# Kernel optimization log

Measured on AMD Instinct MI355X. Metric: run time of the kernel, lower is better.

Reference implementation:

```python
import jax, jax.numpy as jnp
import numpy as np

EMBED = 1024
HEADS = 16
HEAD_DIM = EMBED // HEADS
HIDDEN = 4096
EPS = 1e-6


def _layer_norm(x, gamma, beta):
    mu = jnp.mean(x, axis=-1, keepdims=True)
    var = jnp.mean(jnp.square(x - mu), axis=-1, keepdims=True)
    return (x - mu) * jax.lax.rsqrt(var + EPS) * gamma + beta


def setup_inputs() -> dict:
    key = jax.random.key(0)
    ks = jax.random.split(key, 16)
    s = 1.0 / np.sqrt(EMBED)
    sh = 1.0 / np.sqrt(HIDDEN)
    return {
        "x": jax.random.normal(ks[0], (2, 2048, EMBED), dtype=jnp.float32),
        "Wq": jax.random.uniform(ks[1], (EMBED, EMBED), jnp.float32, -s, s),
        "bq": jnp.zeros((EMBED,), jnp.float32),
        "Wk": jax.random.uniform(ks[2], (EMBED, EMBED), jnp.float32, -s, s),
        "bk": jnp.zeros((EMBED,), jnp.float32),
        "Wv": jax.random.uniform(ks[3], (EMBED, EMBED), jnp.float32, -s, s),
        "bv": jnp.zeros((EMBED,), jnp.float32),
        "Wo": jax.random.uniform(ks[4], (EMBED, EMBED), jnp.float32, -s, s),
        "bo": jnp.zeros((EMBED,), jnp.float32),
        "ln1_g": jnp.ones((EMBED,), jnp.float32),
        "ln1_b": jnp.zeros((EMBED,), jnp.float32),
        "W1": jax.random.uniform(ks[5], (EMBED, HIDDEN), jnp.float32, -s, s),
        "b1": jnp.zeros((HIDDEN,), jnp.float32),
        "W2": jax.random.uniform(ks[6], (HIDDEN, EMBED), jnp.float32, -sh, sh),
        "b2": jnp.zeros((EMBED,), jnp.float32),
        "ln2_g": jnp.ones((EMBED,), jnp.float32),
        "ln2_b": jnp.zeros((EMBED,), jnp.float32),
    }


def reference(x, Wq, bq, Wk, bk, Wv, bv, Wo, bo, ln1_g, ln1_b, W1, b1, W2, b2, ln2_g, ln2_b):
    B, S, _ = x.shape
    # projections (weights stored as [in, out])
    q = (x @ Wq + bq).reshape(B, S, HEADS, HEAD_DIM)
    k = (x @ Wk + bk).reshape(B, S, HEADS, HEAD_DIM)
    v = (x @ Wv + bv).reshape(B, S, HEADS, HEAD_DIM)
    # scores: [B, H, S, S]
    scores = jnp.einsum('bqhd,bkhd->bhqk', q, k) / jnp.sqrt(jnp.float32(HEAD_DIM))
    attn = jax.nn.softmax(scores, axis=-1)
    ctx = jnp.einsum('bhqk,bkhd->bqhd', attn, v).reshape(B, S, EMBED)
    attn_out = ctx @ Wo + bo
    x1 = _layer_norm(x + attn_out, ln1_g, ln1_b)
    ffn = jax.nn.relu(x1 @ W1 + b1) @ W2 + b2
    return _layer_norm(x1 + ffn, ln2_g, ln2_b)
```

## Files before the change

### kernel.cpp

```cpp
#include <hip/hip_runtime.h>
#include <math.h>

#define EMBED 1024
#define HEADS 16
#define HDIM  64
#define HIDDEN 4096
#define BATCH 2
#define SEQ   2048
#define TOK   (BATCH * SEQ)

typedef _Float16 f16;
typedef f16 f16x8 __attribute__((ext_vector_type(8)));
typedef f16 f16x4 __attribute__((ext_vector_type(4)));
typedef f16 f16x2 __attribute__((ext_vector_type(2)));
typedef float f32x4 __attribute__((ext_vector_type(4)));
typedef float f32x16 __attribute__((ext_vector_type(16)));

__device__ __forceinline__ void gload16(const void* g, void* s) {
  __builtin_amdgcn_global_load_lds(
      (const __attribute__((address_space(1))) unsigned int*)g,
      (__attribute__((address_space(3))) unsigned int*)s, 16, 0, 0);
}

template<int A16, int RELU, int OUT16, int QKV>
__global__ __launch_bounds__(256, 2)
void gemm_f16(const void* __restrict__ Av, const f16* __restrict__ Wt,
              const float* __restrict__ bias0, const float* __restrict__ bias1,
              const float* __restrict__ bias2, void* __restrict__ Cv,
              int N, int K, int nbx) {
  __shared__ f16 As[512 * 8];
  __shared__ f16 Bs[512 * 8];
  const int tid = threadIdx.x;
  const int l = tid & 63, w = tid >> 6;
  const int g = l >> 4, ln = l & 15;
  int bid = blockIdx.x;
  const int cpx = gridDim.x >> 3;
  bid = (bid & 7) * cpx + (bid >> 3);
  const int m0 = (bid / nbx) << 7;
  const int n0 = (bid % nbx) << 7;
  const int wr = w >> 1, wc = w & 1;

  f32x4 acc[4][4] = {};

  for (int k0 = 0; k0 < K; k0 += 32) {
    if (A16) {
      const f16* A = (const f16*)Av;
#pragma unroll
      for (int p = 0; p < 2; ++p) {
        const int u0 = p * 256 + w * 64;
        const int ks = u0 >> 7;
        const int row = ((u0 + l) & 127) ^ ks;
        gload16(A + (size_t)(m0 + row) * K + k0 + ks * 8, (void*)&As[u0 * 8]);
      }
    } else {
      const float* A = (const float*)Av;
      const int ks = tid & 3;
      const int r0 = tid >> 2;
#pragma unroll
      for (int p = 0; p < 2; ++p) {
        const int row = r0 + p * 64;
        const float* src = A + (size_t)(m0 + row) * K + k0 + ks * 8;
        float4 f0 = *(const float4*)src;
        float4 f1 = *(const float4*)(src + 4);
        f16x8 hh;
        hh[0] = (f16)f0.x; hh[1] = (f16)f0.y; hh[2] = (f16)f0.z; hh[3] = (f16)f0.w;
        hh[4] = (f16)f1.x; hh[5] = (f16)f1.y; hh[6] = (f16)f1.z; hh[7] = (f16)f1.w;
        *(f16x8*)&As[(ks * 128 + (row ^ ks)) * 8] = hh;
      }
    }
#pragma unroll
    for (int p = 0; p < 2; ++p) {
      const int u0 = p * 256 + w * 64;
      const int ks = u0 >> 7;
      const int col = ((u0 + l) & 127) ^ ks;
      gload16(Wt + (size_t)(n0 + col) * K + k0 + ks * 8, (void*)&Bs[u0 * 8]);
    }
    __syncthreads();
    f16x8 af[4], bf[4];
#pragma unroll
    for (int m = 0; m < 4; ++m)
      af[m] = *(const f16x8*)&As[(g * 128 + ((wr * 64 + m * 16 + ln) ^ g)) * 8];
#pragma unroll
    for (int n = 0; n < 4; ++n)
      bf[n] = *(const f16x8*)&Bs[(g * 128 + ((wc * 64 + n * 16 + ln) ^ g)) * 8];
#pragma unroll
    for (int m = 0; m < 4; ++m)
#pragma unroll
      for (int n = 0; n < 4; ++n)
        acc[m][n] = __builtin_amdgcn_mfma_f32_16x16x32_f16(af[m], bf[n], acc[m][n], 0, 0, 0);
    __syncthreads();
  }

  const float* bp = bias0;
  int nbase = n0;
  float scale = 1.f;
  if (QKV) {
    const int seg = n0 >> 10;
    bp = (seg == 0) ? bias0 : (seg == 1) ? bias1 : bias2;
    nbase = n0 & 1023;
    if (seg == 0) scale = 0.125f * 1.44269504f;
  }
  float bv[4];
#pragma unroll
  for (int n = 0; n < 4; ++n) bv[n] = bp[nbase + wc * 64 + n * 16 + ln];
#pragma unroll
  for (int m = 0; m < 4; ++m)
#pragma unroll
    for (int n = 0; n < 4; ++n)
#pragma unroll
      for (int r = 0; r < 4; ++r) {
        float v = (acc[m][n][r] + bv[n]) * scale;
        if (RELU) v = fmaxf(v, 0.f);
        const size_t idx = (size_t)(m0 + wr * 64 + m * 16 + g * 4 + r) * N
                         + n0 + wc * 64 + n * 16 + ln;
        if (OUT16) ((f16*)Cv)[idx] = (f16)v;
        else       ((float*)Cv)[idx] = v;
      }
}

__device__ __forceinline__ unsigned kchunk(int key, int m) { return (unsigned)(m ^ (key & 7)); }

template<int BASE>
__device__ __forceinline__ f16x8 pack_frag(f32x16 p) {
  f16x8 r;
#pragma unroll
  for (int j = 0; j < 8; ++j) r[j] = (f16)p[BASE + j];
  return r;
}

#define VSTRIDE 68

__global__ __launch_bounds__(256, 2)
void attention(const f16* __restrict__ qkv, f16* __restrict__ ctx) {
  __shared__ f16 Ks[64 * 64];
  __shared__ f16 VT[64 * VSTRIDE];
  const int tid = threadIdx.x;
  const int l = tid & 63, w = tid >> 6;
  const int ln = l & 31, hi = l >> 5;
  const int bh = blockIdx.y, b = bh >> 4, h = bh & 15;
  const int q0 = blockIdx.x * 128;

  f16x8 qf[4];
  {
    const f16* qp = qkv + (size_t)(b * SEQ + q0 + w * 32 + ln) * 3072 + h * 64 + hi * 8;
#pragma unroll
    for (int kc = 0; kc < 4; ++kc) qf[kc] = *(const f16x8*)(qp + kc * 16);
  }

  f32x16 o0 = {}, o1 = {};
  float mrow = -1e30f, lrow = 0.f;

  const int skey = tid >> 3, sc = tid & 7;

  for (int kt = 0; kt < SEQ / 64; ++kt) {
    const size_t tb = (size_t)(b * SEQ + kt * 64) * 3072 + h * 64;
    f16x8 va = *(const f16x8*)(qkv + tb + 2048 + (size_t)skey * 3072 + sc * 8);
    f16x8 vb = *(const f16x8*)(qkv + tb + 2048 + (size_t)(32 + skey) * 3072 + sc * 8);
#pragma unroll
    for (int p = 0; p < 2; ++p) {
      const int key = p * 32 + skey;
      gload16(qkv + tb + 1024 + (size_t)key * 3072 + 8 * kchunk(key, sc),
              (void*)&Ks[(p * 256 + w * 64) * 8]);
    }
#pragma unroll
    for (int j = 0; j < 8; ++j) {
      const int d = sc * 8 + j;
      VT[d * VSTRIDE + skey] = va[j];
      VT[d * VSTRIDE + 32 + skey] = vb[j];
    }
    __syncthreads();

    f32x16 st0 = {}, st1 = {};
#pragma unroll
    for (int kc = 0; kc < 4; ++kc) {
      const int m = kc * 2 + hi;
      const f16x8 kf0 = *(const f16x8*)&Ks[(ln * 8 + (m ^ (ln & 7))) * 8];
      const f16x8 kf1 = *(const f16x8*)&Ks[((32 + ln) * 8 + (m ^ (ln & 7))) * 8];
      st0 = __builtin_amdgcn_mfma_f32_32x32x16_f16(kf0, qf[kc], st0, 0, 0, 0);
      st1 = __builtin_amdgcn_mfma_f32_32x32x16_f16(kf1, qf[kc], st1, 0, 0, 0);
    }

    float mt = st0[0];
#pragma unroll
    for (int r = 1; r < 16; ++r) mt = fmaxf(mt, st0[r]);
#pragma unroll
    for (int r = 0; r < 16; ++r) mt = fmaxf(mt, st1[r]);
    mt = fmaxf(mt, __shfl_xor(mt, 32));
    const float mn = fmaxf(mrow, mt);
    const float al = exp2f(mrow - mn);
    mrow = mn;
    float ps = 0.f;
#pragma unroll
    for (int r = 0; r < 16; ++r) { st0[r] = exp2f(st0[r] - mn); ps += st0[r]; }
#pragma unroll
    for (int r = 0; r < 16; ++r) { st1[r] = exp2f(st1[r] - mn); ps += st1[r]; }
    ps += __shfl_xor(ps, 32);
    lrow = lrow * al + ps;
#pragma unroll
    for (int r = 0; r < 16; ++r) { o0[r] *= al; o1[r] *= al; }

    f16x8 pf[4];
    pf[0] = pack_frag<0>(st0); pf[1] = pack_frag<8>(st0);
    pf[2] = pack_frag<0>(st1); pf[3] = pack_frag<8>(st1);

#pragma unroll
    for (int s = 0; s < 4; ++s) {
      const int k0a = 16 * s + 4 * hi;
      {
        const f16* p0 = &VT[ln * VSTRIDE + k0a];
        f16x4 x = *(const f16x4*)p0;
        f16x4 y = *(const f16x4*)(p0 + 8);
        f16x8 vf = __builtin_shufflevector(x, y, 0, 1, 2, 3, 4, 5, 6, 7);
        o0 = __builtin_amdgcn_mfma_f32_32x32x16_f16(vf, pf[s], o0, 0, 0, 0);
      }
      {
        const f16* p1 = &VT[(32 + ln) * VSTRIDE + k0a];
        f16x4 x = *(const f16x4*)p1;
        f16x4 y = *(const f16x4*)(p1 + 8);
        f16x8 vf = __builtin_shufflevector(x, y, 0, 1, 2, 3, 4, 5, 6, 7);
        o1 = __builtin_amdgcn_mfma_f32_32x32x16_f16(vf, pf[s], o1, 0, 0, 0);
      }
    }
    __syncthreads();
  }

  const float inv = 1.f / lrow;
  f16* cp = ctx + (size_t)(b * SEQ + q0 + w * 32 + ln) * EMBED + h * 64;
#pragma unroll
  for (int r = 0; r < 16; ++r) {
    const int drow = (r & 3) + 8 * (r >> 2) + 4 * hi;
    cp[drow] = (f16)(o0[r] * inv);
    cp[32 + drow] = (f16)(o1[r] * inv);
  }
}

template<int OUT16>
__global__ __launch_bounds__(256, 4)
void add_ln(const float* __restrict__ a, const float* __restrict__ r,
            const float* __restrict__ gam, const float* __restrict__ bet,
            float* __restrict__ out, f16* __restrict__ out16) {
  const int t = blockIdx.x;
  const int tid = threadIdx.x;
  const size_t base = (size_t)t * EMBED + tid * 4;
  float4 av = *(const float4*)(a + base);
  float4 rv = *(const float4*)(r + base);
  const float x0 = av.x + rv.x, x1 = av.y + rv.y;
  const float x2 = av.z + rv.z, x3 = av.w + rv.w;
  float s1 = x0 + x1 + x2 + x3;
  float s2 = x0 * x0 + x1 * x1 + x2 * x2 + x3 * x3;
  for (int off = 1; off < 64; off <<= 1) {
    s1 += __shfl_xor(s1, off);
    s2 += __shfl_xor(s2, off);
  }
  __shared__ float red[8];
  if ((tid & 63) == 0) { red[(tid >> 6) * 2] = s1; red[(tid >> 6) * 2 + 1] = s2; }
  __syncthreads();
  s1 = red[0] + red[2] + red[4] + red[6];
  s2 = red[1] + red[3] + red[5] + red[7];
  const float mu = s1 * (1.f / EMBED);
  const float var = s2 * (1.f / EMBED) - mu * mu;
  const float rstd = rsqrtf(var + 1e-6f);
  float4 gv = *(const float4*)(gam + tid * 4);
  float4 bv = *(const float4*)(bet + tid * 4);
  float4 ov;
  ov.x = (x0 - mu) * rstd * gv.x + bv.x;
  ov.y = (x1 - mu) * rstd * gv.y + bv.y;
  ov.z = (x2 - mu) * rstd * gv.z + bv.z;
  ov.w = (x3 - mu) * rstd * gv.w + bv.w;
  *(float4*)(out + base) = ov;
  if (OUT16) {
    f16x4 hh;
    hh[0] = (f16)ov.x; hh[1] = (f16)ov.y; hh[2] = (f16)ov.z; hh[3] = (f16)ov.w;
    *(f16x4*)(out16 + base) = hh;
  }
}

__global__ __launch_bounds__(256, 4)
void transpose_w(const float* __restrict__ in, f16* __restrict__ out,
                 int K, int N) {
  __shared__ float t[32][33];
  const int tid = threadIdx.x;
  const int k0 = blockIdx.y * 32, n0 = blockIdx.x * 32;
  {
    const int ky = tid >> 3, nx = (tid & 7) * 4;
    float4 f = *(const float4*)(in + (size_t)(k0 + ky) * N + n0 + nx);
    t[ky][nx] = f.x; t[ky][nx + 1] = f.y; t[ky][nx + 2] = f.z; t[ky][nx + 3] = f.w;
  }
  __syncthreads();
  const int ny = tid >> 3, kx = (tid & 7) * 4;
  f16x4 hh;
  hh[0] = (f16)t[kx][ny];     hh[1] = (f16)t[kx + 1][ny];
  hh[2] = (f16)t[kx + 2][ny]; hh[3] = (f16)t[kx + 3][ny];
  *(f16x4*)(out + (size_t)(n0 + ny) * K + k0 + kx) = hh;
}

extern "C" void kernel_launch(void* const* d_in, const int* in_sizes, int n_in,
                              void* d_out, int out_size, void* d_ws, size_t ws_size,
                              hipStream_t stream) {
  const float* x    = (const float*)d_in[0];
  const float* Wq   = (const float*)d_in[1];
  const float* bq   = (const float*)d_in[2];
  const float* Wk   = (const float*)d_in[3];
  const float* bk   = (const float*)d_in[4];
  const float* Wv   = (const float*)d_in[5];
  const float* bv   = (const float*)d_in[6];
  const float* Wo   = (const float*)d_in[7];
  const float* bo   = (const float*)d_in[8];
  const float* ln1g = (const float*)d_in[9];
  const float* ln1b = (const float*)d_in[10];
  const float* W1   = (const float*)d_in[11];
  const float* b1   = (const float*)d_in[12];
  const float* W2   = (const float*)d_in[13];
  const float* b2   = (const float*)d_in[14];
  const float* ln2g = (const float*)d_in[15];
  const float* ln2b = (const float*)d_in[16];
  float* out = (float*)d_out;

  char* ws = (char*)d_ws;
  const size_t MB = 1024 * 1024;
  f16*   WtQKV = (f16*)(ws);
  f16*   WtO   = (f16*)(ws + 6 * MB);
  f16*   Wt1   = (f16*)(ws + 8 * MB);
  f16*   Wt2   = (f16*)(ws + 16 * MB);
  f16*   qkv   = (f16*)(ws + 24 * MB);
  f16*   ctx   = (f16*)(ws + 48 * MB);
  float* ao    = (float*)(ws + 56 * MB);
  float* x1    = (float*)(ws + 72 * MB);
  f16*   x1h   = (f16*)(ws + 88 * MB);
  f16*   hid   = (f16*)(ws + 24 * MB);
  float* ffn   = ao;

  const dim3 blk(256);
  transpose_w<<<dim3(32, 32), blk, 0, stream>>>(Wq, WtQKV, 1024, 1024);
  transpose_w<<<dim3(32, 32), blk, 0, stream>>>(Wk, WtQKV + 1024 * 1024, 1024, 1024);
  transpose_w<<<dim3(32, 32), blk, 0, stream>>>(Wv, WtQKV + 2 * 1024 * 1024, 1024, 1024);
  transpose_w<<<dim3(32, 32), blk, 0, stream>>>(Wo, WtO, 1024, 1024);
  transpose_w<<<dim3(128, 32), blk, 0, stream>>>(W1, Wt1, 1024, 4096);
  transpose_w<<<dim3(32, 128), blk, 0, stream>>>(W2, Wt2, 4096, 1024);

  gemm_f16<0, 0, 1, 1><<<768, blk, 0, stream>>>(x, WtQKV, bq, bk, bv, qkv, 3072, 1024, 24);
  attention<<<dim3(16, 32), blk, 0, stream>>>(qkv, ctx);
  gemm_f16<1, 0, 0, 0><<<256, blk, 0, stream>>>(ctx, WtO, bo, nullptr, nullptr, ao, 1024, 1024, 8);
  add_ln<1><<<4096, blk, 0, stream>>>(x, ao, ln1g, ln1b, x1, x1h);
  gemm_f16<1, 1, 1, 0><<<1024, blk, 0, stream>>>(x1h, Wt1, b1, nullptr, nullptr, hid, 4096, 1024, 32);
  gemm_f16<1, 0, 0, 0><<<256, blk, 0, stream>>>(hid, Wt2, b2, nullptr, nullptr, ffn, 1024, 4096, 8);
  add_ln<0><<<4096, blk, 0, stream>>>(x1, ffn, ln2g, ln2b, out, nullptr);
}
```

Baseline: 502.0 us.

## Split-K the N=1024 GEMMs and fold partial sums plus bias into add+LayerNorm

The Wo and W2 projections only produce 256 tiles of 128x128, which underfills the GPU. They now run as split-K with 2 slices (512 blocks), and each slice writes fp32 partials to the workspace. The add_ln kernel sums the partials, the bias and the residual before normalising. It also merges the three QKV weight transposes into one launch, raises the launch-bounds occupancy hint from 2 to 3, and writes x1 into the output buffer instead of a separate workspace region. The cost is extra fp32 partial-sum traffic and possible register pressure from the higher occupancy target.

```diff
diff --git a/kernel.cpp b/kernel.cpp
--- a/kernel.cpp
+++ b/kernel.cpp
@@ -12,7 +12,6 @@
 typedef _Float16 f16;
 typedef f16 f16x8 __attribute__((ext_vector_type(8)));
 typedef f16 f16x4 __attribute__((ext_vector_type(4)));
-typedef f16 f16x2 __attribute__((ext_vector_type(2)));
 typedef float f32x4 __attribute__((ext_vector_type(4)));
 typedef float f32x16 __attribute__((ext_vector_type(16)));
 
@@ -22,8 +21,8 @@
       (__attribute__((address_space(3))) unsigned int*)s, 16, 0, 0);
 }
 
-template<int A16, int RELU, int OUT16, int QKV>
-__global__ __launch_bounds__(256, 2)
+template<int A16, int RELU, int OUT16, int QKV, int SPLITK>
+__global__ __launch_bounds__(256, 3)
 void gemm_f16(const void* __restrict__ Av, const f16* __restrict__ Wt,
               const float* __restrict__ bias0, const float* __restrict__ bias1,
               const float* __restrict__ bias2, void* __restrict__ Cv,
@@ -34,15 +33,20 @@
   const int l = tid & 63, w = tid >> 6;
   const int g = l >> 4, ln = l & 15;
   int bid = blockIdx.x;
-  const int cpx = gridDim.x >> 3;
+  int slice = 0;
+  if (SPLITK > 1) { slice = bid % SPLITK; bid /= SPLITK; }
+  const int ntiles = gridDim.x / SPLITK;
+  const int cpx = ntiles >> 3;
   bid = (bid & 7) * cpx + (bid >> 3);
   const int m0 = (bid / nbx) << 7;
   const int n0 = (bid % nbx) << 7;
   const int wr = w >> 1, wc = w & 1;
+  const int ksl = K / SPLITK;
+  const int kbeg = slice * ksl, kend = kbeg + ksl;
 
   f32x4 acc[4][4] = {};
 
-  for (int k0 = 0; k0 < K; k0 += 32) {
+  for (int k0 = kbeg; k0 < kend; k0 += 32) {
     if (A16) {
       const f16* A = (const f16*)Av;
 #pragma unroll
@@ -91,6 +95,21 @@
     __syncthreads();
   }
 
+  if (SPLITK > 1) {
+    float* P = (float*)Cv + (size_t)slice * TOK * N;
+#pragma unroll
+    for (int m = 0; m < 4; ++m)
+#pragma unroll
+      for (int n = 0; n < 4; ++n)
+#pragma unroll
+        for (int r = 0; r < 4; ++r) {
+          const size_t idx = (size_t)(m0 + wr * 64 + m * 16 + g * 4 + r) * N
+                           + n0 + wc * 64 + n * 16 + ln;
+          P[idx] = acc[m][n][r];
+        }
+    return;
+  }
+
   const float* bp = bias0;
   int nbase = n0;
   float scale = 1.f;
@@ -234,18 +253,22 @@
   }
 }
 
-template<int OUT16>
+template<int NP, int OUT16>
 __global__ __launch_bounds__(256, 4)
-void add_ln(const float* __restrict__ a, const float* __restrict__ r,
-            const float* __restrict__ gam, const float* __restrict__ bet,
-            float* __restrict__ out, f16* __restrict__ out16) {
+void add_ln(const float* parts, const float* __restrict__ bias,
+            const float* resid, const float* __restrict__ gam,
+            const float* __restrict__ bet, float* out, f16* __restrict__ out16) {
   const int t = blockIdx.x;
   const int tid = threadIdx.x;
   const size_t base = (size_t)t * EMBED + tid * 4;
-  float4 av = *(const float4*)(a + base);
-  float4 rv = *(const float4*)(r + base);
-  const float x0 = av.x + rv.x, x1 = av.y + rv.y;
-  const float x2 = av.z + rv.z, x3 = av.w + rv.w;
+  float4 rv = *(const float4*)(resid + base);
+  float4 bb = *(const float4*)(bias + tid * 4);
+  float x0 = rv.x + bb.x, x1 = rv.y + bb.y, x2 = rv.z + bb.z, x3 = rv.w + bb.w;
+#pragma unroll
+  for (int p = 0; p < NP; ++p) {
+    float4 pv = *(const float4*)(parts + (size_t)p * TOK * EMBED + base);
+    x0 += pv.x; x1 += pv.y; x2 += pv.z; x3 += pv.w;
+  }
   float s1 = x0 + x1 + x2 + x3;
   float s2 = x0 * x0 + x1 * x1 + x2 * x2 + x3 * x3;
   for (int off = 1; off < 64; off <<= 1) {
@@ -275,12 +298,9 @@
   }
 }
 
-__global__ __launch_bounds__(256, 4)
-void transpose_w(const float* __restrict__ in, f16* __restrict__ out,
-                 int K, int N) {
+__device__ __forceinline__ void transpose_tile(const float* in, f16* out,
+                                               int K, int N, int k0, int n0, int tid) {
   __shared__ float t[32][33];
-  const int tid = threadIdx.x;
-  const int k0 = blockIdx.y * 32, n0 = blockIdx.x * 32;
   {
     const int ky = tid >> 3, nx = (tid & 7) * 4;
     float4 f = *(const float4*)(in + (size_t)(k0 + ky) * N + n0 + nx);
@@ -292,6 +312,20 @@
   hh[0] = (f16)t[kx][ny];     hh[1] = (f16)t[kx + 1][ny];
   hh[2] = (f16)t[kx + 2][ny]; hh[3] = (f16)t[kx + 3][ny];
   *(f16x4*)(out + (size_t)(n0 + ny) * K + k0 + kx) = hh;
+}
+
+__global__ __launch_bounds__(256, 4)
+void transpose_w(const float* __restrict__ in, f16* __restrict__ out,
+                 int K, int N) {
+  transpose_tile(in, out, K, N, blockIdx.y * 32, blockIdx.x * 32, threadIdx.x);
+}
+
+__global__ __launch_bounds__(256, 4)
+void transpose_qkv(const float* __restrict__ w0, const float* __restrict__ w1,
+                   const float* __restrict__ w2, f16* __restrict__ out) {
+  const float* in = (blockIdx.z == 0) ? w0 : (blockIdx.z == 1) ? w1 : w2;
+  f16* o = out + (size_t)blockIdx.z * 1024 * 1024;
+  transpose_tile(in, o, 1024, 1024, blockIdx.y * 32, blockIdx.x * 32, threadIdx.x);
 }
 
 extern "C" void kernel_launch(void* const* d_in, const int* in_sizes, int n_in,
@@ -324,25 +358,22 @@
   f16*   Wt2   = (f16*)(ws + 16 * MB);
   f16*   qkv   = (f16*)(ws + 24 * MB);
   f16*   ctx   = (f16*)(ws + 48 * MB);
-  float* ao    = (float*)(ws + 56 * MB);
-  float* x1    = (float*)(ws + 72 * MB);
+  float* parts = (float*)(ws + 56 * MB);
   f16*   x1h   = (f16*)(ws + 88 * MB);
   f16*   hid   = (f16*)(ws + 24 * MB);
-  float* ffn   = ao;
+  float* x1    = out;
 
   const dim3 blk(256);
-  transpose_w<<<dim3(32, 32), blk, 0, stream>>>(Wq, WtQKV, 1024, 1024);
-  transpose_w<<<dim3(32, 32), blk, 0, stream>>>(Wk, WtQKV + 1024 * 1024, 1024, 1024);
-  transpose_w<<<dim3(32, 32), blk, 0, stream>>>(Wv, WtQKV + 2 * 1024 * 1024, 1024, 1024);
+  transpose_qkv<<<dim3(32, 32, 3), blk, 0, stream>>>(Wq, Wk, Wv, WtQKV);
   transpose_w<<<dim3(32, 32), blk, 0, stream>>>(Wo, WtO, 1024, 1024);
   transpose_w<<<dim3(128, 32), blk, 0, stream>>>(W1, Wt1, 1024, 4096);
   transpose_w<<<dim3(32, 128), blk, 0, stream>>>(W2, Wt2, 4096, 1024);
 
-  gemm_f16<0, 0, 1, 1><<<768, blk, 0, stream>>>(x, WtQKV, bq, bk, bv, qkv, 3072, 1024, 24);
+  gemm_f16<0, 0, 1, 1, 1><<<768, blk, 0, stream>>>(x, WtQKV, bq, bk, bv, qkv, 3072, 1024, 24);
   attention<<<dim3(16, 32), blk, 0, stream>>>(qkv, ctx);
-  gemm_f16<1, 0, 0, 0><<<256, blk, 0, stream>>>(ctx, WtO, bo, nullptr, nullptr, ao, 1024, 1024, 8);
-  add_ln<1><<<4096, blk, 0, stream>>>(x, ao, ln1g, ln1b, x1, x1h);
-  gemm_f16<1, 1, 1, 0><<<1024, blk, 0, stream>>>(x1h, Wt1, b1, nullptr, nullptr, hid, 4096, 1024, 32);
-  gemm_f16<1, 0, 0, 0><<<256, blk, 0, stream>>>(hid, Wt2, b2, nullptr, nullptr, ffn, 1024, 4096, 8);
-  add_ln<0><<<4096, blk, 0, stream>>>(x1, ffn, ln2g, ln2b, out, nullptr);
-}
+  gemm_f16<1, 0, 0, 0, 2><<<512, blk, 0, stream>>>(ctx, WtO, nullptr, nullptr, nullptr, parts, 1024, 1024, 8);
+  add_ln<2, 1><<<4096, blk, 0, stream>>>(parts, bo, x, ln1g, ln1b, x1, x1h);
+  gemm_f16<1, 1, 1, 0, 1><<<1024, blk, 0, stream>>>(x1h, Wt1, b1, nullptr, nullptr, hid, 4096, 1024, 32);
+  gemm_f16<1, 0, 0, 0, 2><<<512, blk, 0, stream>>>(hid, Wt2, nullptr, nullptr, nullptr, parts, 1024, 4096, 8);
+  add_ln<2, 0><<<4096, blk, 0, stream>>>(parts, b2, x1, ln2g, ln2b, out, nullptr);
+}
```

Measured after the change: 451.7 us. 1.11x faster.
